# Kernel optimization log

Hardware: AMD Instinct MI355X
Metric: run time of the kernel (lower is better)

## Reference

```python
import jax, jax.numpy as jnp
import numpy as np

BS, IN_CH, SEQ = 2, 512, 1024
DK, DV, H = 64, 64, 16


def setup_inputs() -> dict:
    key = jax.random.key(0)
    ks = jax.random.split(key, 8)
    # init scales mirror the torch init lambdas
    sq = IN_CH ** (-0.5) * DK ** (-0.25)            # initQ / initK
    sv = (1.0 / 0.012) * H ** (-0.5) * IN_CH ** (-0.5) * 40 ** (-0.5)  # initV
    sl = 0.5 * H ** (-0.5)                           # initL
    inp = jax.random.normal(ks[0], (BS, IN_CH, SEQ), jnp.float32)
    mask = jnp.zeros((BS, SEQ), jnp.float32)
    Wq = jax.random.normal(ks[1], (IN_CH, DK, H), jnp.float32) * sq
    Wk = jax.random.normal(ks[2], (IN_CH, DK, H), jnp.float32) * sq
    Wv = jax.random.normal(ks[3], (IN_CH, DV, H), jnp.float32) * sv
    Wl = jax.random.normal(ks[4], (H, H), jnp.float32) * sl
    Ww = jax.random.normal(ks[5], (H, H), jnp.float32) * 0.01
    Wo = jax.random.normal(ks[6], (DV * H, IN_CH), jnp.float32) * 0.03
    alpha = jnp.full((1,), 2.0, jnp.float32)
    return {"inp": inp, "mask": mask, "Wq": Wq, "Wk": Wk, "Wv": Wv,
            "alphaq": alpha, "alphak": alpha, "alphav": alpha,
            "Wl": Wl, "Ww": Ww, "Wo": Wo}


def reference(inp, mask, Wq, Wk, Wv, alphaq, alphak, alphav, Wl, Ww, Wo):
    # inp: (b, c_in, s); projections -> (b, d, s, h)
    Q = jax.nn.sigmoid(alphaq) * jnp.einsum('bcs,cdh->bdsh', inp, Wq)
    K = jax.nn.sigmoid(alphak) * jnp.einsum('bcs,cdh->bdsh', inp, Wk)
    V = jax.nn.sigmoid(alphav) * jnp.einsum('bcs,cdh->bdsh', inp, Wv)
    # per-head attention logits: (b, sq, sk, h)
    J = jnp.einsum('bdqh,bdkh->bqkh', Q, K)
    # pre-softmax head mixing, additive mask over key positions
    EL = jnp.einsum('bqkh,hg->bqkg', J, Wl) - mask[:, None, :, None]
    W = jax.nn.softmax(EL, axis=2)  # softmax over keys (dim 2)
    # post-softmax head mixing
    U = jnp.einsum('bqkg,gv->bqkv', W, Ww)
    # attend to values: (b, sq, dv, hv) -> (b, sq, dv*hv)
    O = jnp.einsum('bqkv,bdkv->bqdv', U, V)
    O = O.reshape(O.shape[0], O.shape[1], DV * H)
    # output projection, back to (b, out_dim, s)
    resid = jnp.einsum('bqc,cd->bdq', O, Wo)
    # shortcut is identity since out_dim == in_ch
    return inp + resid
```

## Files before the change

kernel.cpp:

```cpp
#include <hip/hip_runtime.h>
#include <hip/hip_bf16.h>


#define B_S  2
#define C_INN 512
#define SEQL 1024
#define D_K  64
#define N_H  16
#define BQJ  (2 * 1024 * 1024)
#define KSL  16
#define KSO  8

typedef __attribute__((ext_vector_type(4))) float floatx4;
typedef __attribute__((ext_vector_type(8))) short short8;
typedef __attribute__((ext_vector_type(2))) unsigned int uint2v;
typedef __fp16 h2raw __attribute__((ext_vector_type(2)));
typedef _Float16 f16x4 __attribute__((ext_vector_type(4)));

static __device__ __forceinline__ float bf2f(unsigned short u) {
  union { unsigned int i; float f; } x; x.i = ((unsigned int)u) << 16; return x.f;
}
static __device__ __forceinline__ unsigned short f2bf(float f) {
  union { float f; unsigned int i; } x; x.f = f;
  return (unsigned short)((x.i + 0x7fffu + ((x.i >> 16) & 1u)) >> 16);
}
static __device__ __forceinline__ unsigned int pkh2(float a, float b) {
  h2raw r = __builtin_amdgcn_cvt_pkrtz(a, b);
  union { h2raw h; unsigned int u; } x; x.h = r; return x.u;
}
static __device__ __forceinline__ unsigned int pkbf(float a, float b) {
  return (unsigned int)f2bf(a) | ((unsigned int)f2bf(b) << 16);
}
static __device__ __forceinline__ f16x4 mkh4(unsigned int a, unsigned int b) {
  union { unsigned int u[2]; f16x4 h; } x; x.u[0] = a; x.u[1] = b; return x.h;
}

__global__ __launch_bounds__(256) void ath_tr(
    const float* __restrict__ inp, const float* __restrict__ Wq,
    const float* __restrict__ Wk,  const float* __restrict__ Wv,
    const float* __restrict__ Wo,
    unsigned short* __restrict__ inpT, unsigned short* __restrict__ WT,
    unsigned short* __restrict__ WoT)
{
  const int z = blockIdx.z;
  const float* src; unsigned short* dst; int R, C;
  if      (z == 0) { src = inp;              dst = inpT;                R = 512;  C = 1024; }
  else if (z == 1) { src = inp + 512 * 1024; dst = inpT + 1024 * 512;   R = 512;  C = 1024; }
  else if (z == 2) { src = Wq;               dst = WT;                  R = 512;  C = 1024; }
  else if (z == 3) { src = Wk;               dst = WT + 1024 * 512;     R = 512;  C = 1024; }
  else if (z == 4) { src = Wv;               dst = WT + 2 * 1024 * 512; R = 512;  C = 1024; }
  else             { src = Wo;               dst = WoT;                 R = 1024; C = 512;  }
  const int ct = blockIdx.x, rt = blockIdx.y;
  if (ct * 32 >= C || rt * 32 >= R) return;

  __shared__ float Ts[32][33];
  const int t = threadIdx.x;
  {
    const int r = t >> 3, c4 = (t & 7) * 4;
    const floatx4 g = *(const floatx4*)(src + (size_t)(rt * 32 + r) * C + ct * 32 + c4);
    Ts[r][c4 + 0] = g[0]; Ts[r][c4 + 1] = g[1];
    Ts[r][c4 + 2] = g[2]; Ts[r][c4 + 3] = g[3];
  }
  __syncthreads();
  {
    const int i = t >> 3, k4 = (t & 7) * 4;
    const unsigned int o0 = pkbf(Ts[k4 + 0][i], Ts[k4 + 1][i]);
    const unsigned int o1 = pkbf(Ts[k4 + 2][i], Ts[k4 + 3][i]);
    *(uint2v*)(dst + (size_t)(ct * 32 + i) * R + rt * 32 + k4) = (uint2v){o0, o1};
  }
}

__global__ __launch_bounds__(256) void ath_qkv(
    const unsigned short* __restrict__ inpT,
    const unsigned short* __restrict__ WT,
    const float* __restrict__ Aq,
    const float* __restrict__ Ak,
    const float* __restrict__ Av,
    unsigned short* __restrict__ ws)
{
  const int sblk = blockIdx.x;
  const int nblk = blockIdx.y;
  const int z = blockIdx.z;
  const int b = z / 3, p = z % 3;
  const float* Ap = (p == 0) ? Aq : ((p == 1) ? Ak : Av);
  const float sig = 1.0f / (1.0f + __expf(-Ap[0]));

  __shared__ __align__(16) unsigned short As[64][40];
  __shared__ __align__(16) unsigned short Bs[64][40];

  const int tid = threadIdx.x;
  const int w = tid >> 6, lane = tid & 63;
  const int l15 = lane & 15, quad = lane >> 4;
  const int srow = tid >> 2, sc8 = (tid & 3) * 8;

  floatx4 acc[4];
#pragma unroll
  for (int i = 0; i < 4; ++i) acc[i] = (floatx4){0.f, 0.f, 0.f, 0.f};

  for (int cc = 0; cc < 16; ++cc) {
    const int c0 = cc * 32;
    __syncthreads();
    *(short8*)&As[srow][sc8] =
        *(const short8*)(inpT + ((size_t)(b * 1024 + sblk * 64 + srow)) * 512 + c0 + sc8);
    *(short8*)&Bs[srow][sc8] =
        *(const short8*)(WT + ((size_t)(p * 1024 + nblk * 64 + srow)) * 512 + c0 + sc8);
    __syncthreads();
    const short8 a = *(const short8*)&As[w * 16 + l15][quad * 8];
#pragma unroll
    for (int nt = 0; nt < 4; ++nt) {
      const short8 bb = *(const short8*)&Bs[nt * 16 + l15][quad * 8];
      acc[nt] = __builtin_amdgcn_mfma_f32_16x16x32_bf16(a, bb, acc[nt], 0, 0, 0);
    }
  }

  unsigned short* out = ws + (size_t)p * ((size_t)B_S * N_H * SEQL * D_K);
#pragma unroll
  for (int nt = 0; nt < 4; ++nt) {
    const int h = l15;
    const int d = nblk * 4 + nt;
#pragma unroll
    for (int r = 0; r < 4; ++r) {
      const int s = sblk * 64 + w * 16 + quad * 4 + r;
      const float vout = acc[nt][r] * sig;
      if (p == 2) out[((size_t)((b * N_H + h) * D_K + d)) * SEQL + s] = f2bf(vout);
      else        out[((size_t)((b * N_H + h) * SEQL + s)) * D_K + d] = f2bf(vout);
    }
  }
}

__global__ __launch_bounds__(256, 3) void ath_lpart(
    const float* __restrict__ maskp,
    const float* __restrict__ Wl,
    const unsigned short* __restrict__ qkv,
    float* __restrict__ lp)
{
  const int qblk = blockIdx.x;
  const int ks   = blockIdx.y;
  const int b    = blockIdx.z;
  const int tid = threadIdx.x;
  const int w = tid >> 6, lane = tid & 63;
  const int l15 = lane & 15, quad = lane >> 4;

  const unsigned short* Qf = qkv;
  const unsigned short* Kf = qkv + (size_t)B_S * N_H * SEQL * D_K;

  __shared__ unsigned int JtU[9216];

  const f16x4 wlA = mkh4(pkh2(Wl[(quad * 4 + 0) * 16 + l15], Wl[(quad * 4 + 1) * 16 + l15]),
                         pkh2(Wl[(quad * 4 + 2) * 16 + l15], Wl[(quad * 4 + 3) * 16 + l15]));
  const f16x4 idB = mkh4(pkh2((quad * 4 + 0 == l15) ? 1.f : 0.f, (quad * 4 + 1 == l15) ? 1.f : 0.f),
                         pkh2((quad * 4 + 2 == l15) ? 1.f : 0.f, (quad * 4 + 3 == l15) ? 1.f : 0.f));
  const unsigned int ONE2 = 0x3C003C00u;
  const f16x4 onesB = mkh4(ONE2, ONE2);
  const f16x4 zeroB = mkh4(0u, 0u);

  const float mreg = maskp[b * SEQL + ks * 64 + w * 16 + l15];
  const int k0 = ks * 64;

  short8 qf0[4], qf1[4];
#pragma unroll
  for (int hh = 0; hh < 4; ++hh) {
    const unsigned short* qb =
        Qf + ((size_t)((b * N_H + w * 4 + hh) * SEQL) + qblk * 16 + l15) * D_K;
    qf0[hh] = *(const short8*)(qb + quad * 8);
    qf1[hh] = *(const short8*)(qb + 32 + quad * 8);
  }

#pragma unroll
  for (int kt = 0; kt < 4; ++kt) {
    floatx4 jc[4];
#pragma unroll
    for (int hh = 0; hh < 4; ++hh) {
      const unsigned short* kb =
          Kf + ((size_t)((b * N_H + w * 4 + hh) * SEQL) + k0 + kt * 16 + l15) * D_K;
      const short8 kf0 = *(const short8*)(kb + quad * 8);
      const short8 kf1 = *(const short8*)(kb + 32 + quad * 8);
      floatx4 c = (floatx4){0.f, 0.f, 0.f, 0.f};
      c = __builtin_amdgcn_mfma_f32_16x16x32_bf16(qf0[hh], kf0, c, 0, 0, 0);
      c = __builtin_amdgcn_mfma_f32_16x16x32_bf16(qf1[hh], kf1, c, 0, 0, 0);
      jc[hh] = c;
    }
#pragma unroll
    for (int r = 0; r < 4; ++r) {
      const int base = ((quad * 4 + r) * 64 + kt * 16 + l15) * 9 + w * 2;
      JtU[base + 0] = pkh2(jc[0][r], jc[1][r]);
      JtU[base + 1] = pkh2(jc[2][r], jc[3][r]);
    }
  }

  __syncthreads();

  floatx4 dl0 = (floatx4){0.f, 0.f, 0.f, 0.f};
  floatx4 dl1 = (floatx4){0.f, 0.f, 0.f, 0.f};
#pragma unroll 4
  for (int q = 0; q < 16; ++q) {
    const int jb = (q * 64 + w * 16 + l15) * 9 + quad * 2;
    const f16x4 bj = mkh4(JtU[jb], JtU[jb + 1]);
    floatx4 d1 = __builtin_amdgcn_mfma_f32_16x16x16f16(
        wlA, bj, (floatx4){0.f, 0.f, 0.f, 0.f}, 0, 0, 0);
    float p[4];
#pragma unroll
    for (int r = 0; r < 4; ++r) {
      const float e = fminf(fmaxf(d1[r] - mreg, -60.f), 60.f);
      p[r] = __expf(e);
    }
    const f16x4 ap = mkh4(pkh2(p[0], p[1]), pkh2(p[2], p[3]));
    floatx4 dt = __builtin_amdgcn_mfma_f32_16x16x16f16(
        ap, idB, (floatx4){0.f, 0.f, 0.f, 0.f}, 0, 0, 0);
    const f16x4 a2 = mkh4(pkh2(dt[0], dt[1]), pkh2(dt[2], dt[3]));
    const f16x4 eq = (l15 == q) ? onesB : zeroB;
    if (q & 1) dl1 = __builtin_amdgcn_mfma_f32_16x16x16f16(a2, eq, dl1, 0, 0, 0);
    else       dl0 = __builtin_amdgcn_mfma_f32_16x16x16f16(a2, eq, dl0, 0, 0, 0);
  }
  const floatx4 dl = dl0 + dl1;

  *(floatx4*)(lp + ((size_t)((ks * 4 + w) * 2 + b)) * 16384 +
              (size_t)(qblk * 16 + l15) * 16 + quad * 4) = dl;
}

__global__ __launch_bounds__(256) void ath_linv(
    const float* __restrict__ lp, float* __restrict__ invl)
{
  const int t = blockIdx.x * 256 + threadIdx.x;
  const int b = t >> 14, rem = t & 16383;
  float s = 0.f;
#pragma unroll
  for (int sl = 0; sl < KSL * 4; ++sl) s += lp[(size_t)(sl * 2 + b) * 16384 + rem];
  invl[t] = 1.0f / fmaxf(s, 1e-37f);
}

__global__ __launch_bounds__(256, 2) void ath_opart(
    const float* __restrict__ maskp,
    const float* __restrict__ Wl,
    const float* __restrict__ Ww,
    const unsigned short* __restrict__ qkv,
    const float* __restrict__ invl,
    unsigned short* __restrict__ Obp)
{
  const int qblk = blockIdx.x;
  const int ks   = blockIdx.y;
  const int b    = blockIdx.z;
  const int tid = threadIdx.x;
  const int w = tid >> 6, lane = tid & 63;
  const int l15 = lane & 15, quad = lane >> 4;

  const unsigned short* Qf = qkv;
  const unsigned short* Kf = qkv + (size_t)B_S * N_H * SEQL * D_K;
  const unsigned short* Vf = qkv + 2 * (size_t)B_S * N_H * SEQL * D_K;

  __shared__ unsigned int JtU[9216];
  __shared__ __align__(16) unsigned short Us[16 * 16 * 64];
  __shared__ float invls[16][16];

  invls[tid >> 4][tid & 15] =
      invl[(size_t)b * 16384 + (qblk * 16 + (tid >> 4)) * 16 + (tid & 15)];

  const f16x4 wlA = mkh4(pkh2(Wl[(quad * 4 + 0) * 16 + l15], Wl[(quad * 4 + 1) * 16 + l15]),
                         pkh2(Wl[(quad * 4 + 2) * 16 + l15], Wl[(quad * 4 + 3) * 16 + l15]));
  const f16x4 wwB = mkh4(pkh2(Ww[(quad * 4 + 0) * 16 + l15], Ww[(quad * 4 + 1) * 16 + l15]),
                         pkh2(Ww[(quad * 4 + 2) * 16 + l15], Ww[(quad * 4 + 3) * 16 + l15]));

  short8 qf0[4], qf1[4];
#pragma unroll
  for (int hh = 0; hh < 4; ++hh) {
    const unsigned short* qb =
        Qf + ((size_t)((b * N_H + w * 4 + hh) * SEQL) + qblk * 16 + l15) * D_K;
    qf0[hh] = *(const short8*)(qb + quad * 8);
    qf1[hh] = *(const short8*)(qb + 32 + quad * 8);
  }

  floatx4 oacc[4][4];
#pragma unroll
  for (int a = 0; a < 4; ++a)
#pragma unroll
    for (int d = 0; d < 4; ++d) oacc[a][d] = (floatx4){0.f, 0.f, 0.f, 0.f};

  __syncthreads();

  for (int rd = 0; rd < 2; ++rd) {
    const int k0 = ks * 128 + rd * 64;
    const float mreg = maskp[b * SEQL + k0 + w * 16 + l15];

#pragma unroll
    for (int kt = 0; kt < 4; ++kt) {
      floatx4 jc[4];
#pragma unroll
      for (int hh = 0; hh < 4; ++hh) {
        const unsigned short* kb =
            Kf + ((size_t)((b * N_H + w * 4 + hh) * SEQL) + k0 + kt * 16 + l15) * D_K;
        const short8 kf0 = *(const short8*)(kb + quad * 8);
        const short8 kf1 = *(const short8*)(kb + 32 + quad * 8);
        floatx4 c = (floatx4){0.f, 0.f, 0.f, 0.f};
        c = __builtin_amdgcn_mfma_f32_16x16x32_bf16(qf0[hh], kf0, c, 0, 0, 0);
        c = __builtin_amdgcn_mfma_f32_16x16x32_bf16(qf1[hh], kf1, c, 0, 0, 0);
        jc[hh] = c;
      }
#pragma unroll
      for (int r = 0; r < 4; ++r) {
        const int base = ((quad * 4 + r) * 64 + kt * 16 + l15) * 9 + w * 2;
        JtU[base + 0] = pkh2(jc[0][r], jc[1][r]);
        JtU[base + 1] = pkh2(jc[2][r], jc[3][r]);
      }
    }

    __syncthreads();

#pragma unroll 4
    for (int q = 0; q < 16; ++q) {
      const int jb = (q * 64 + w * 16 + l15) * 9 + quad * 2;
      const f16x4 bj = mkh4(JtU[jb], JtU[jb + 1]);
      floatx4 d1 = __builtin_amdgcn_mfma_f32_16x16x16f16(
          wlA, bj, (floatx4){0.f, 0.f, 0.f, 0.f}, 0, 0, 0);
      const floatx4 iq = *(const floatx4*)&invls[q][quad * 4];
      float p[4];
#pragma unroll
      for (int r = 0; r < 4; ++r) {
        const float e = fminf(fmaxf(d1[r] - mreg, -60.f), 60.f);
        p[r] = __expf(e) * iq[r];
      }
      const f16x4 ap = mkh4(pkh2(p[0], p[1]), pkh2(p[2], p[3]));
      floatx4 d2 = __builtin_amdgcn_mfma_f32_16x16x16f16(
          ap, wwB, (floatx4){0.f, 0.f, 0.f, 0.f}, 0, 0, 0);
      const int row = l15 * 16 + q;
      const int ch = (w * 2 + (quad >> 1)) ^ ((l15 ^ q) & 7);
      *(uint2v*)&Us[row * 64 + ch * 8 + (quad & 1) * 4] =
          (uint2v){pkbf(d2[0], d2[1]), pkbf(d2[2], d2[3])};
    }

    __syncthreads();

#pragma unroll
    for (int tp = 0; tp < 2; ++tp) {
      const int kt_abs = ks * 128 + rd * 64 + tp * 32;
#pragma unroll
      for (int vv = 0; vv < 4; ++vv) {
        const int v = w * 4 + vv;
        const int ch = (tp * 4 + quad) ^ ((v ^ l15) & 7);
        const short8 ufr = *(const short8*)&Us[(v * 16 + l15) * 64 + ch * 8];
#pragma unroll
        for (int dt = 0; dt < 4; ++dt) {
          const short8 vfr = *(const short8*)(Vf +
              ((size_t)((b * N_H + v) * D_K + dt * 16 + l15)) * SEQL + kt_abs + quad * 8);
          oacc[vv][dt] = __builtin_amdgcn_mfma_f32_16x16x32_bf16(ufr, vfr, oacc[vv][dt], 0, 0, 0);
        }
      }
    }

    __syncthreads();
  }

#pragma unroll
  for (int vv = 0; vv < 4; ++vv) {
    const int v = w * 4 + vv;
#pragma unroll
    for (int dt = 0; dt < 4; ++dt) {
      const int d = dt * 16 + l15;
#pragma unroll
      for (int r = 0; r < 4; ++r) {
        const int q = qblk * 16 + quad * 4 + r;
        Obp[(size_t)ks * BQJ + ((size_t)(b * SEQL + q)) * 1024 + d * 16 + v] = f2bf(oacc[vv][dt][r]);
      }
    }
  }
}

__global__ __launch_bounds__(256) void ath_osum(
    const unsigned short* __restrict__ Obp,
    unsigned short* __restrict__ Obsum)
{
  const size_t i = ((size_t)blockIdx.x * 256 + threadIdx.x) * 8;
  float a[8];
#pragma unroll
  for (int e = 0; e < 8; ++e) a[e] = 0.f;
#pragma unroll
  for (int ks = 0; ks < KSO; ++ks) {
    const short8 v = *(const short8*)(Obp + (size_t)ks * BQJ + i);
#pragma unroll
    for (int e = 0; e < 8; ++e) a[e] += bf2f((unsigned short)v[e]);
  }
  short8 o;
#pragma unroll
  for (int e = 0; e < 8; ++e) o[e] = (short)f2bf(a[e]);
  *(short8*)(Obsum + i) = o;
}

__global__ __launch_bounds__(256) void ath_out(
    const float* __restrict__ inp,
    const unsigned short* __restrict__ WoT,
    const unsigned short* __restrict__ Ob,
    float* __restrict__ out)
{
  const int qblk = blockIdx.x;
  const int cblk = blockIdx.y;
  const int b    = blockIdx.z;
  const int tid = threadIdx.x;
  const int w = tid >> 6, lane = tid & 63;
  const int l15 = lane & 15, quad = lane >> 4;

  __shared__ __align__(16) unsigned short Os[64][40];
  __shared__ __align__(16) unsigned short Wt[64][40];

  floatx4 acc[4];
#pragma unroll
  for (int i = 0; i < 4; ++i) acc[i] = (floatx4){0.f, 0.f, 0.f, 0.f};

  const int srow = tid >> 2, sj8 = (tid & 3) * 8;

  for (int jc = 0; jc < 32; ++jc) {
    const int j0 = jc * 32;
    __syncthreads();
    *(short8*)&Os[srow][sj8] =
        *(const short8*)(Ob + ((size_t)(b * SEQL + qblk * 64 + srow)) * 1024 + j0 + sj8);
    *(short8*)&Wt[srow][sj8] =
        *(const short8*)(WoT + ((size_t)(cblk * 64 + srow)) * 1024 + j0 + sj8);
    __syncthreads();
    const short8 a = *(const short8*)&Os[w * 16 + l15][quad * 8];
#pragma unroll
    for (int nt = 0; nt < 4; ++nt) {
      const short8 bb = *(const short8*)&Wt[nt * 16 + l15][quad * 8];
      acc[nt] = __builtin_amdgcn_mfma_f32_16x16x32_bf16(a, bb, acc[nt], 0, 0, 0);
    }
  }

#pragma unroll
  for (int nt = 0; nt < 4; ++nt) {
    const int co = cblk * 64 + nt * 16 + l15;
    const int qb = qblk * 64 + w * 16 + quad * 4;
    const float* ip = inp + ((size_t)(b * 512 + co)) * SEQL + qb;
    float* op = out + ((size_t)(b * 512 + co)) * SEQL + qb;
#pragma unroll
    for (int r = 0; r < 4; ++r) op[r] = acc[nt][r] + ip[r];
  }
}

extern "C" void kernel_launch(void* const* d_in, const int* in_sizes, int n_in,
                              void* d_out, int out_size, void* d_ws, size_t ws_size,
                              hipStream_t stream) {
  (void)in_sizes; (void)n_in; (void)out_size; (void)ws_size;
  const float* inp   = (const float*)d_in[0];
  const float* maskp = (const float*)d_in[1];
  const float* Wq    = (const float*)d_in[2];
  const float* Wk    = (const float*)d_in[3];
  const float* Wv    = (const float*)d_in[4];
  const float* Aq    = (const float*)d_in[5];
  const float* Ak    = (const float*)d_in[6];
  const float* Av    = (const float*)d_in[7];
  const float* Wl    = (const float*)d_in[8];
  const float* Ww    = (const float*)d_in[9];
  const float* Wo    = (const float*)d_in[10];

  const size_t MB = 1u << 20;
  unsigned short* qkv   = (unsigned short*)d_ws;
  unsigned short* Obsum = (unsigned short*)((char*)d_ws + 12 * MB);
  float*          invl  = (float*)((char*)d_ws + 16 * MB);
  unsigned short* WoT   = (unsigned short*)((char*)d_ws + 17 * MB);
  float*          lp    = (float*)((char*)d_ws + 18 * MB);
  unsigned short* WT    = (unsigned short*)((char*)d_ws + 26 * MB);
  unsigned short* inpT  = (unsigned short*)((char*)d_ws + 29 * MB);
  unsigned short* Obp   = (unsigned short*)((char*)d_ws + 18 * MB);
  float* out = (float*)d_out;

  ath_tr<<<dim3(32, 32, 6), 256, 0, stream>>>(inp, Wq, Wk, Wv, Wo, inpT, WT, WoT);
  ath_qkv<<<dim3(16, 16, 6), 256, 0, stream>>>(inpT, WT, Aq, Ak, Av, qkv);
  ath_lpart<<<dim3(64, KSL, 2), 256, 0, stream>>>(maskp, Wl, qkv, lp);
  ath_linv<<<dim3(128), 256, 0, stream>>>(lp, invl);
  ath_opart<<<dim3(64, KSO, 2), 256, 0, stream>>>(maskp, Wl, Ww, qkv, invl, Obp);
  ath_osum<<<dim3(1024), 256, 0, stream>>>(Obp, Obsum);
  ath_out<<<dim3(16, 8, 2), 256, 0, stream>>>(inp, WoT, Obsum, out);
}
```

Measured before the change: 269.1 us.

## Materialize exp probabilities in workspace to skip QK recompute in output pass

The normalization pass now also writes the unnormalized exp(EL) values as fp16 to a 64 MB workspace buffer. A new output-pass kernel reads them back instead of recomputing QK^T, the Wl mixing and the exp, and goes straight to the Ww mixing and the V product. This swaps recomputation for a large round trip through HBM. The path only runs when the workspace is at least 114 MB. The fallback output kernel also reuses the JtU shared buffer for U in place of a separate Us buffer, which cuts LDS use.

```diff
diff --git a/kernel.cpp b/kernel.cpp
--- a/kernel.cpp
+++ b/kernel.cpp
@@ -128,11 +128,12 @@
   }
 }
 
-__global__ __launch_bounds__(256, 3) void ath_lpart(
+__global__ __launch_bounds__(256, 3) void ath_lpartP(
     const float* __restrict__ maskp,
     const float* __restrict__ Wl,
     const unsigned short* __restrict__ qkv,
-    float* __restrict__ lp)
+    float* __restrict__ lp,
+    unsigned short* __restrict__ Pws)
 {
   const int qblk = blockIdx.x;
   const int ks   = blockIdx.y;
@@ -156,6 +157,7 @@
 
   const float mreg = maskp[b * SEQL + ks * 64 + w * 16 + l15];
   const int k0 = ks * 64;
+  const int kabs = k0 + w * 16 + l15;
 
   short8 qf0[4], qf1[4];
 #pragma unroll
@@ -190,6 +192,7 @@
 
   __syncthreads();
 
+  unsigned int* Pu = (unsigned int*)Pws;
   floatx4 dl0 = (floatx4){0.f, 0.f, 0.f, 0.f};
   floatx4 dl1 = (floatx4){0.f, 0.f, 0.f, 0.f};
 #pragma unroll 4
@@ -204,6 +207,102 @@
       const float e = fminf(fmaxf(d1[r] - mreg, -60.f), 60.f);
       p[r] = __expf(e);
     }
+    const unsigned int u0 = pkh2(p[0], p[1]);
+    const unsigned int u1 = pkh2(p[2], p[3]);
+    const size_t pidx =
+        ((size_t)(b * 1024 + qblk * 16 + q) * 1024 + kabs) * 8 + quad * 2;
+    *(uint2v*)&Pu[pidx] = (uint2v){u0, u1};
+
+    const f16x4 ap = mkh4(u0, u1);
+    floatx4 dt = __builtin_amdgcn_mfma_f32_16x16x16f16(
+        ap, idB, (floatx4){0.f, 0.f, 0.f, 0.f}, 0, 0, 0);
+    const f16x4 a2 = mkh4(pkh2(dt[0], dt[1]), pkh2(dt[2], dt[3]));
+    const f16x4 eq = (l15 == q) ? onesB : zeroB;
+    if (q & 1) dl1 = __builtin_amdgcn_mfma_f32_16x16x16f16(a2, eq, dl1, 0, 0, 0);
+    else       dl0 = __builtin_amdgcn_mfma_f32_16x16x16f16(a2, eq, dl0, 0, 0, 0);
+  }
+  const floatx4 dl = dl0 + dl1;
+
+  *(floatx4*)(lp + ((size_t)((ks * 4 + w) * 2 + b)) * 16384 +
+              (size_t)(qblk * 16 + l15) * 16 + quad * 4) = dl;
+}
+
+__global__ __launch_bounds__(256, 3) void ath_lpart(
+    const float* __restrict__ maskp,
+    const float* __restrict__ Wl,
+    const unsigned short* __restrict__ qkv,
+    float* __restrict__ lp)
+{
+  const int qblk = blockIdx.x;
+  const int ks   = blockIdx.y;
+  const int b    = blockIdx.z;
+  const int tid = threadIdx.x;
+  const int w = tid >> 6, lane = tid & 63;
+  const int l15 = lane & 15, quad = lane >> 4;
+
+  const unsigned short* Qf = qkv;
+  const unsigned short* Kf = qkv + (size_t)B_S * N_H * SEQL * D_K;
+
+  __shared__ unsigned int JtU[9216];
+
+  const f16x4 wlA = mkh4(pkh2(Wl[(quad * 4 + 0) * 16 + l15], Wl[(quad * 4 + 1) * 16 + l15]),
+                         pkh2(Wl[(quad * 4 + 2) * 16 + l15], Wl[(quad * 4 + 3) * 16 + l15]));
+  const f16x4 idB = mkh4(pkh2((quad * 4 + 0 == l15) ? 1.f : 0.f, (quad * 4 + 1 == l15) ? 1.f : 0.f),
+                         pkh2((quad * 4 + 2 == l15) ? 1.f : 0.f, (quad * 4 + 3 == l15) ? 1.f : 0.f));
+  const unsigned int ONE2 = 0x3C003C00u;
+  const f16x4 onesB = mkh4(ONE2, ONE2);
+  const f16x4 zeroB = mkh4(0u, 0u);
+
+  const float mreg = maskp[b * SEQL + ks * 64 + w * 16 + l15];
+  const int k0 = ks * 64;
+
+  short8 qf0[4], qf1[4];
+#pragma unroll
+  for (int hh = 0; hh < 4; ++hh) {
+    const unsigned short* qb =
+        Qf + ((size_t)((b * N_H + w * 4 + hh) * SEQL) + qblk * 16 + l15) * D_K;
+    qf0[hh] = *(const short8*)(qb + quad * 8);
+    qf1[hh] = *(const short8*)(qb + 32 + quad * 8);
+  }
+
+#pragma unroll
+  for (int kt = 0; kt < 4; ++kt) {
+    floatx4 jc[4];
+#pragma unroll
+    for (int hh = 0; hh < 4; ++hh) {
+      const unsigned short* kb =
+          Kf + ((size_t)((b * N_H + w * 4 + hh) * SEQL) + k0 + kt * 16 + l15) * D_K;
+      const short8 kf0 = *(const short8*)(kb + quad * 8);
+      const short8 kf1 = *(const short8*)(kb + 32 + quad * 8);
+      floatx4 c = (floatx4){0.f, 0.f, 0.f, 0.f};
+      c = __builtin_amdgcn_mfma_f32_16x16x32_bf16(qf0[hh], kf0, c, 0, 0, 0);
+      c = __builtin_amdgcn_mfma_f32_16x16x32_bf16(qf1[hh], kf1, c, 0, 0, 0);
+      jc[hh] = c;
+    }
+#pragma unroll
+    for (int r = 0; r < 4; ++r) {
+      const int base = ((quad * 4 + r) * 64 + kt * 16 + l15) * 9 + w * 2;
+      JtU[base + 0] = pkh2(jc[0][r], jc[1][r]);
+      JtU[base + 1] = pkh2(jc[2][r], jc[3][r]);
+    }
+  }
+
+  __syncthreads();
+
+  floatx4 dl0 = (floatx4){0.f, 0.f, 0.f, 0.f};
+  floatx4 dl1 = (floatx4){0.f, 0.f, 0.f, 0.f};
+#pragma unroll 4
+  for (int q = 0; q < 16; ++q) {
+    const int jb = (q * 64 + w * 16 + l15) * 9 + quad * 2;
+    const f16x4 bj = mkh4(JtU[jb], JtU[jb + 1]);
+    floatx4 d1 = __builtin_amdgcn_mfma_f32_16x16x16f16(
+        wlA, bj, (floatx4){0.f, 0.f, 0.f, 0.f}, 0, 0, 0);
+    float p[4];
+#pragma unroll
+    for (int r = 0; r < 4; ++r) {
+      const float e = fminf(fmaxf(d1[r] - mreg, -60.f), 60.f);
+      p[r] = __expf(e);
+    }
     const f16x4 ap = mkh4(pkh2(p[0], p[1]), pkh2(p[2], p[3]));
     floatx4 dt = __builtin_amdgcn_mfma_f32_16x16x16f16(
         ap, idB, (floatx4){0.f, 0.f, 0.f, 0.f}, 0, 0, 0);
@@ -229,6 +328,107 @@
   invl[t] = 1.0f / fmaxf(s, 1e-37f);
 }
 
+__global__ __launch_bounds__(256, 2) void ath_opartP(
+    const unsigned short* __restrict__ Pws,
+    const float* __restrict__ Ww,
+    const unsigned short* __restrict__ qkv,
+    const float* __restrict__ invl,
+    unsigned short* __restrict__ Obp)
+{
+  const int qblk = blockIdx.x;
+  const int ks   = blockIdx.y;
+  const int b    = blockIdx.z;
+  const int tid = threadIdx.x;
+  const int w = tid >> 6, lane = tid & 63;
+  const int l15 = lane & 15, quad = lane >> 4;
+
+  const unsigned short* Vf = qkv + 2 * (size_t)B_S * N_H * SEQL * D_K;
+
+  __shared__ __align__(16) unsigned short Us[16 * 16 * 64];
+  __shared__ float invls[16][16];
+
+  invls[tid >> 4][tid & 15] =
+      invl[(size_t)b * 16384 + (qblk * 16 + (tid >> 4)) * 16 + (tid & 15)];
+
+  const f16x4 wwB = mkh4(pkh2(Ww[(quad * 4 + 0) * 16 + l15], Ww[(quad * 4 + 1) * 16 + l15]),
+                         pkh2(Ww[(quad * 4 + 2) * 16 + l15], Ww[(quad * 4 + 3) * 16 + l15]));
+
+  floatx4 oacc[4][4];
+#pragma unroll
+  for (int a = 0; a < 4; ++a)
+#pragma unroll
+    for (int d = 0; d < 4; ++d) oacc[a][d] = (floatx4){0.f, 0.f, 0.f, 0.f};
+
+  const unsigned int* Pu = (const unsigned int*)Pws;
+
+  __syncthreads();
+
+  for (int rd = 0; rd < 2; ++rd) {
+    const int kabs = ks * 128 + rd * 64 + w * 16 + l15;
+
+#pragma unroll
+    for (int qh = 0; qh < 2; ++qh) {
+      uint2v pv[8];
+#pragma unroll
+      for (int qq = 0; qq < 8; ++qq) {
+        const size_t pidx =
+            ((size_t)(b * 1024 + qblk * 16 + qh * 8 + qq) * 1024 + kabs) * 8 + quad * 2;
+        pv[qq] = *(const uint2v*)&Pu[pidx];
+      }
+#pragma unroll
+      for (int qq = 0; qq < 8; ++qq) {
+        const int q = qh * 8 + qq;
+        const floatx4 iq = *(const floatx4*)&invls[q][quad * 4];
+        union { unsigned int u; _Float16 h[2]; } z0, z1;
+        z0.u = pv[qq][0]; z1.u = pv[qq][1];
+        const f16x4 ap = mkh4(pkh2((float)z0.h[0] * iq[0], (float)z0.h[1] * iq[1]),
+                              pkh2((float)z1.h[0] * iq[2], (float)z1.h[1] * iq[3]));
+        floatx4 d2 = __builtin_amdgcn_mfma_f32_16x16x16f16(
+            ap, wwB, (floatx4){0.f, 0.f, 0.f, 0.f}, 0, 0, 0);
+        const int row = l15 * 16 + q;
+        const int ch = (w * 2 + (quad >> 1)) ^ ((l15 ^ q) & 7);
+        *(uint2v*)&Us[row * 64 + ch * 8 + (quad & 1) * 4] =
+            (uint2v){pkbf(d2[0], d2[1]), pkbf(d2[2], d2[3])};
+      }
+    }
+
+    __syncthreads();
+
+#pragma unroll
+    for (int tp = 0; tp < 2; ++tp) {
+      const int kt_abs = ks * 128 + rd * 64 + tp * 32;
+#pragma unroll
+      for (int vv = 0; vv < 4; ++vv) {
+        const int v = w * 4 + vv;
+        const int ch = (tp * 4 + quad) ^ ((v ^ l15) & 7);
+        const short8 ufr = *(const short8*)&Us[(v * 16 + l15) * 64 + ch * 8];
+#pragma unroll
+        for (int dt = 0; dt < 4; ++dt) {
+          const short8 vfr = *(const short8*)(Vf +
+              ((size_t)((b * N_H + v) * D_K + dt * 16 + l15)) * SEQL + kt_abs + quad * 8);
+          oacc[vv][dt] = __builtin_amdgcn_mfma_f32_16x16x32_bf16(ufr, vfr, oacc[vv][dt], 0, 0, 0);
+        }
+      }
+    }
+
+    __syncthreads();
+  }
+
+#pragma unroll
+  for (int vv = 0; vv < 4; ++vv) {
+    const int v = w * 4 + vv;
+#pragma unroll
+    for (int dt = 0; dt < 4; ++dt) {
+      const int d = dt * 16 + l15;
+#pragma unroll
+      for (int r = 0; r < 4; ++r) {
+        const int q = qblk * 16 + quad * 4 + r;
+        Obp[(size_t)ks * BQJ + ((size_t)(b * SEQL + q)) * 1024 + d * 16 + v] = f2bf(oacc[vv][dt][r]);
+      }
+    }
+  }
+}
+
 __global__ __launch_bounds__(256, 2) void ath_opart(
     const float* __restrict__ maskp,
     const float* __restrict__ Wl,
@@ -249,7 +449,6 @@
   const unsigned short* Vf = qkv + 2 * (size_t)B_S * N_H * SEQL * D_K;
 
   __shared__ unsigned int JtU[9216];
-  __shared__ __align__(16) unsigned short Us[16 * 16 * 64];
   __shared__ float invls[16][16];
 
   invls[tid >> 4][tid & 15] =
@@ -321,22 +520,22 @@
       const f16x4 ap = mkh4(pkh2(p[0], p[1]), pkh2(p[2], p[3]));
       floatx4 d2 = __builtin_amdgcn_mfma_f32_16x16x16f16(
           ap, wwB, (floatx4){0.f, 0.f, 0.f, 0.f}, 0, 0, 0);
-      const int row = l15 * 16 + q;
-      const int ch = (w * 2 + (quad >> 1)) ^ ((l15 ^ q) & 7);
-      *(uint2v*)&Us[row * 64 + ch * 8 + (quad & 1) * 4] =
-          (uint2v){pkbf(d2[0], d2[1]), pkbf(d2[2], d2[3])};
-    }
-
-    __syncthreads();
-
+      const int ub = (q * 64 + w * 16) * 9 + ((l15 + q) & 15) * 8 + quad * 2;
+      *(uint2v*)&JtU[ub] = (uint2v){pkbf(d2[0], d2[1]), pkbf(d2[2], d2[3])};
+    }
+
+    __syncthreads();
+
+    const unsigned short* JtS = (const unsigned short*)JtU;
 #pragma unroll
     for (int tp = 0; tp < 2; ++tp) {
       const int kt_abs = ks * 128 + rd * 64 + tp * 32;
 #pragma unroll
       for (int vv = 0; vv < 4; ++vv) {
         const int v = w * 4 + vv;
-        const int ch = (tp * 4 + quad) ^ ((v ^ l15) & 7);
-        const short8 ufr = *(const short8*)&Us[(v * 16 + l15) * 64 + ch * 8];
+        const int wp = tp * 2 + (quad >> 1);
+        const int so = (l15 * 64 + wp * 16) * 18 + ((v + l15) & 15) * 16 + (quad & 1) * 8;
+        const short8 ufr = *(const short8*)&JtS[so];
 #pragma unroll
         for (int dt = 0; dt < 4; ++dt) {
           const short8 vfr = *(const short8*)(Vf +
@@ -436,7 +635,7 @@
 extern "C" void kernel_launch(void* const* d_in, const int* in_sizes, int n_in,
                               void* d_out, int out_size, void* d_ws, size_t ws_size,
                               hipStream_t stream) {
-  (void)in_sizes; (void)n_in; (void)out_size; (void)ws_size;
+  (void)in_sizes; (void)n_in; (void)out_size;
   const float* inp   = (const float*)d_in[0];
   const float* maskp = (const float*)d_in[1];
   const float* Wq    = (const float*)d_in[2];
@@ -458,13 +657,22 @@
   unsigned short* WT    = (unsigned short*)((char*)d_ws + 26 * MB);
   unsigned short* inpT  = (unsigned short*)((char*)d_ws + 29 * MB);
   unsigned short* Obp   = (unsigned short*)((char*)d_ws + 18 * MB);
+  unsigned short* Pws   = (unsigned short*)((char*)d_ws + 50 * MB);
   float* out = (float*)d_out;
+
+  const bool useP = ws_size >= (size_t)114 * MB;
 
   ath_tr<<<dim3(32, 32, 6), 256, 0, stream>>>(inp, Wq, Wk, Wv, Wo, inpT, WT, WoT);
   ath_qkv<<<dim3(16, 16, 6), 256, 0, stream>>>(inpT, WT, Aq, Ak, Av, qkv);
-  ath_lpart<<<dim3(64, KSL, 2), 256, 0, stream>>>(maskp, Wl, qkv, lp);
-  ath_linv<<<dim3(128), 256, 0, stream>>>(lp, invl);
-  ath_opart<<<dim3(64, KSO, 2), 256, 0, stream>>>(maskp, Wl, Ww, qkv, invl, Obp);
+  if (useP) {
+    ath_lpartP<<<dim3(64, KSL, 2), 256, 0, stream>>>(maskp, Wl, qkv, lp, Pws);
+    ath_linv<<<dim3(128), 256, 0, stream>>>(lp, invl);
+    ath_opartP<<<dim3(64, KSO, 2), 256, 0, stream>>>(Pws, Ww, qkv, invl, Obp);
+  } else {
+    ath_lpart<<<dim3(64, KSL, 2), 256, 0, stream>>>(maskp, Wl, qkv, lp);
+    ath_linv<<<dim3(128), 256, 0, stream>>>(lp, invl);
+    ath_opart<<<dim3(64, KSO, 2), 256, 0, stream>>>(maskp, Wl, Ww, qkv, invl, Obp);
+  }
   ath_osum<<<dim3(1024), 256, 0, stream>>>(Obp, Obsum);
   ath_out<<<dim3(16, 8, 2), 256, 0, stream>>>(inp, WoT, Obsum, out);
 }
```

New measurement: 255.4 us. 5.1% less time.
